# Kernel optimization log

Hardware: AMD Instinct MI355X
Metric: run time of the kernel (lower is better)

Reference implementation:

```python
import jax, jax.numpy as jnp
import numpy as np

B, HW, E = 64, 14, 512   # batch, feature-map side, encoder_dim
A = D = M = 512          # attention_dim, decoder_dim, embed_dim
V = 1000                 # vocab_size
L = 257                  # max caption length -> T = 256 decode steps


def setup_inputs() -> dict:
    key = jax.random.key(0)
    ks = jax.random.split(key, 16)
    def w(k, shape, s=0.05):
        return jax.random.normal(k, shape, dtype=jnp.float32) * s
    encoder_out = jax.random.normal(ks[0], (B, HW, HW, E), dtype=jnp.float32)
    encoded_captions = jax.random.randint(ks[1], (B, L), 0, V)
    caption_lengths = jax.random.randint(ks[2], (B, 1), 2, L + 1)
    caption_lengths = caption_lengths.at[0, 0].set(L)  # ensure max(decode_lengths) == L-1
    return dict(
        encoder_out=encoder_out,
        encoded_captions=encoded_captions,
        caption_lengths=caption_lengths,
        emb=w(ks[3], (V, M), 0.1),
        enc_att_w=w(ks[4], (A, E)), enc_att_b=jnp.zeros((A,), jnp.float32),
        dec_att_w=w(ks[5], (A, D)), dec_att_b=jnp.zeros((A,), jnp.float32),
        full_att_w=w(ks[6], (1, A)), full_att_b=jnp.zeros((1,), jnp.float32),
        W_ih=w(ks[7], (4 * D, M + E)), b_ih=jnp.zeros((4 * D,), jnp.float32),
        W_hh=w(ks[8], (4 * D, D)), b_hh=jnp.zeros((4 * D,), jnp.float32),
        init_h_w=w(ks[9], (D, E)), init_h_b=jnp.zeros((D,), jnp.float32),
        init_c_w=w(ks[10], (D, E)), init_c_b=jnp.zeros((D,), jnp.float32),
        f_beta_w=w(ks[11], (E, D)), f_beta_b=jnp.zeros((E,), jnp.float32),
        fc_w=w(ks[12], (V, D), 0.1), fc_b=jnp.zeros((V,), jnp.float32),
    )


def _forward(encoder_out, emb, enc_att_w, enc_att_b, dec_att_w, dec_att_b,
             full_att_w, full_att_b, W_ih, b_ih, W_hh, b_hh,
             init_h_w, init_h_b, init_c_w, init_c_b,
             f_beta_w, f_beta_b, fc_w, fc_b,
             encoded_captions, caption_lengths):
    Bn = encoder_out.shape[0]
    En = encoder_out.shape[-1]
    enc = encoder_out.reshape(Bn, -1, En)            # [B, P, E]
    lens = caption_lengths[:, 0]
    sort_ind = jnp.argsort(-lens)                    # descending caption length
    lens = lens[sort_ind]
    enc = enc[sort_ind]
    caps = encoded_captions[sort_ind]
    embs = emb[caps]                                 # [B, L, M]
    mean_enc = enc.mean(axis=1)
    h0 = mean_enc @ init_h_w.T + init_h_b            # [B, D]
    c0 = mean_enc @ init_c_w.T + init_c_b
    att1 = enc @ enc_att_w.T + enc_att_b             # [B, P, A] (loop-invariant)
    dec_len = lens - 1
    T = caps.shape[1] - 1
    embs_seq = jnp.transpose(embs[:, :T, :], (1, 0, 2))  # [T, B, M]

    def step(carry, xs):
        h, c = carry
        t, emb_t = xs
        # soft attention (full batch; torch slices to active rows, masked below)
        att2 = h @ dec_att_w.T + dec_att_b                                   # [B, A]
        e = jnp.einsum('bpa,a->bp', jax.nn.relu(att1 + att2[:, None, :]),
                       full_att_w[0]) + full_att_b[0]                        # [B, P]
        alpha = jax.nn.softmax(e, axis=1)
        awe = jnp.einsum('bpe,bp->be', enc, alpha)                           # [B, E]
        gate = jax.nn.sigmoid(h @ f_beta_w.T + f_beta_b)
        x = jnp.concatenate([emb_t, gate * awe], axis=1)                     # [B, M+E]
        # LSTMCell
        gates = x @ W_ih.T + b_ih + h @ W_hh.T + b_hh
        i, f, g, o = jnp.split(gates, 4, axis=1)
        c_new = jax.nn.sigmoid(f) * c + jax.nn.sigmoid(i) * jnp.tanh(g)
        h_new = jax.nn.sigmoid(o) * jnp.tanh(c_new)
        m = (t < dec_len).astype(h.dtype)[:, None]                           # active mask
        h2 = m * h_new + (1 - m) * h
        c2 = m * c_new + (1 - m) * c
        preds = (h_new @ fc_w.T + fc_b) * m   # dropout is identity in eval
        return (h2, c2), (preds, alpha * m)

    (_, _), (preds, alphas) = jax.lax.scan(step, (h0, c0), (jnp.arange(T), embs_seq))
    predictions = jnp.transpose(preds, (1, 0, 2))   # [B, T, V]
    alphas = jnp.transpose(alphas, (1, 0, 2))       # [B, T, P]
    return predictions, caps, alphas, sort_ind


def reference(encoder_out, encoded_captions, caption_lengths, emb,
              enc_att_w, enc_att_b, dec_att_w, dec_att_b, full_att_w, full_att_b,
              W_ih, b_ih, W_hh, b_hh, init_h_w, init_h_b, init_c_w, init_c_b,
              f_beta_w, f_beta_b, fc_w, fc_b):
    return _forward(encoder_out, emb, enc_att_w, enc_att_b, dec_att_w, dec_att_b,
                    full_att_w, full_att_b, W_ih, b_ih, W_hh, b_hh,
                    init_h_w, init_h_b, init_c_w, init_c_b,
                    f_beta_w, f_beta_b, fc_w, fc_b,
                    encoded_captions, caption_lengths)
```

## Files before the change

kernel.cpp:

```cpp
#include <hip/hip_runtime.h>
#include <cstdint>
#include <cstddef>

#define NBLK 256
#define NTHR 512
#define B_ 64
#define P_ 196
#define E_ 512
#define A_ 512
#define D_ 512
#define M_ 512
#define V_ 1000
#define L_ 257
#define T_ 256

#define OUT_PRED  0
#define OUT_CAPS  (B_*T_*V_)
#define OUT_ALPHA (OUT_CAPS + B_*L_)
#define OUT_SORT  (OUT_ALPHA + B_*T_*P_)

typedef _Float16 h2 __attribute__((ext_vector_type(2)));
typedef _Float16 f16x8 __attribute__((ext_vector_type(8)));
typedef float f32x4 __attribute__((ext_vector_type(4)));

struct KP {
  const float* enc; const int* caps; const int* clen;
  const float* emb;
  const float* eaw; const float* eab;
  const float* daw; const float* dab;
  const float* faw; const float* fab;
  const float* wih; const float* bih;
  const float* whh; const float* bhh;
  const float* ihw; const float* ihb;
  const float* icw; const float* icb;
  const float* fbw; const float* fbb;
  const float* fcw; const float* fcb;
  float* out;
  int* bar; int* flb; int* gf;
  int* sort_ind; int* dec_len;
  float* mnT;
  unsigned* hfA; unsigned* hfB; unsigned* hfN;
  float* a2G; float* gateG; float* aweQ; float* sA; float* att1;
};

__device__ __forceinline__ float sigf(float x){ return 1.f/(1.f+__expf(-x)); }
__device__ __forceinline__ float tanhf_(float x){
  float ax = fabsf(x);
  float e = __expf(-2.f*ax);
  float r = (1.f-e)/(1.f+e);
  return x < 0.f ? -r : r;
}
__device__ __forceinline__ unsigned short f2bf(float x){
  unsigned u = __float_as_uint(x);
  unsigned r = (u + 0x7fffu + ((u >> 16) & 1u)) >> 16;
  return (unsigned short)r;
}
__device__ __forceinline__ float fdot2f(h2 a, h2 b, float c){
#if __has_builtin(__builtin_amdgcn_fdot2)
  return __builtin_amdgcn_fdot2(a, b, c, false);
#else
  return c + (float)a.x*(float)b.x + (float)a.y*(float)b.y;
#endif
}
__device__ __forceinline__ unsigned packh2(float a, float b){
  h2 v; v.x = (_Float16)a; v.y = (_Float16)b;
  return __builtin_bit_cast(unsigned, v);
}
__device__ __forceinline__ h2 ash2(unsigned u){ return __builtin_bit_cast(h2, u); }
__device__ __forceinline__ f16x8 asf8(uint4 u){ return __builtin_bit_cast(f16x8, u); }

#define LD_A(p)     __hip_atomic_load((p), __ATOMIC_RELAXED, __HIP_MEMORY_SCOPE_AGENT)
#define ST_A(p,v)   __hip_atomic_store((p),(v), __ATOMIC_RELAXED, __HIP_MEMORY_SCOPE_AGENT)
#define ST_REL(p,v) __hip_atomic_store((p),(v), __ATOMIC_RELEASE, __HIP_MEMORY_SCOPE_AGENT)
#define FAA(p)      __hip_atomic_fetch_add((p),1, __ATOMIC_RELAXED, __HIP_MEMORY_SCOPE_AGENT)
__device__ __forceinline__ float ldg_c(const float* p){
  return __hip_atomic_load(p, __ATOMIC_RELAXED, __HIP_MEMORY_SCOPE_AGENT);
}
__device__ __forceinline__ float2 ldg2_c(const float* p){
  unsigned long long u = __hip_atomic_load((const unsigned long long*)p,
                       __ATOMIC_RELAXED, __HIP_MEMORY_SCOPE_AGENT);
  return __builtin_bit_cast(float2, u);
}
__device__ __forceinline__ uint2 ldgu2_c(const unsigned* p){
  unsigned long long u = __hip_atomic_load((const unsigned long long*)p,
                       __ATOMIC_RELAXED, __HIP_MEMORY_SCOPE_AGENT);
  return __builtin_bit_cast(uint2, u);
}
__device__ __forceinline__ void stg_c(float* p, float v){
  __hip_atomic_store(p, v, __ATOMIC_RELAXED, __HIP_MEMORY_SCOPE_AGENT);
}
__device__ __forceinline__ void stgu_c(unsigned* p, unsigned v){
  __hip_atomic_store(p, v, __ATOMIC_RELAXED, __HIP_MEMORY_SCOPE_AGENT);
}
__device__ __forceinline__ void stg2_c(float* p, float a, float b){
  float2 v; v.x = a; v.y = b;
  __hip_atomic_store((unsigned long long*)p,
                     __builtin_bit_cast(unsigned long long, v),
                     __ATOMIC_RELAXED, __HIP_MEMORY_SCOPE_AGENT);
}

__device__ __forceinline__ void gridbar(int* bar, int blk){
  __syncthreads();
  if (threadIdx.x == 0){
    __builtin_amdgcn_fence(__ATOMIC_RELEASE, "agent");
    int s = LD_A(&bar[144]);
    int* leaf = &bar[(blk & 7)*16];
    if (FAA(leaf) == 31){
      ST_A(leaf, 0);
      if (FAA(&bar[128]) == 7){
        ST_A(&bar[128], 0);
        ST_REL(&bar[144], s+1);
      }
    }
    while (LD_A(&bar[144]) == s) __builtin_amdgcn_s_sleep(2);
    __builtin_amdgcn_fence(__ATOMIC_ACQUIRE, "agent");
  }
  __syncthreads();
}

__device__ __forceinline__ void octbar(int* fl, int O, int r, int ep){
  __syncthreads();
  if (threadIdx.x == 0) ST_A(&fl[O*64 + r], ep);
  if (threadIdx.x < 32){
    while (LD_A(&fl[O*64 + (int)threadIdx.x]) < ep) __builtin_amdgcn_s_sleep(1);
  }
  asm volatile("" ::: "memory");
  __syncthreads();
}

#define REDW_STORE() do { \
  const int j = lane & 15; \
  if (j < 8){ \
    const int ib = (lane >> 4) * 4; \
    _Pragma("unroll") \
    for (int r = 0; r < 4; r++){ \
      redW[wave*512 + (( 0 + ib + r)*8) + j] = d0[r]; \
      redW[wave*512 + ((16 + ib + r)*8) + j] = d1[r]; \
      redW[wave*512 + ((32 + ib + r)*8) + j] = d2[r]; \
      redW[wave*512 + ((48 + ib + r)*8) + j] = d3[r]; \
    } \
  } \
} while(0)

template<int KSW>
__device__ __forceinline__ void gemv_regs(const uint4 (&wfr)[4][KSW],
                                          const uint4* __restrict__ x4,
                                          float* redW, int lane, int wave){
  f32x4 d0 = {0.f,0.f,0.f,0.f}, d1 = d0, d2 = d0, d3 = d0;
  const int rowc = lane & 7;
  const int lg = lane >> 4;
  #pragma unroll
  for (int ks = 0; ks < KSW; ks++){
    const int ksg = wave*KSW + ks;
    f16x8 bf = asf8(x4[(ksg*4 + lg)*8 + rowc]);
    d0 = __builtin_amdgcn_mfma_f32_16x16x32_f16(asf8(wfr[0][ks]), bf, d0, 0, 0, 0);
    d1 = __builtin_amdgcn_mfma_f32_16x16x32_f16(asf8(wfr[1][ks]), bf, d1, 0, 0, 0);
    d2 = __builtin_amdgcn_mfma_f32_16x16x32_f16(asf8(wfr[2][ks]), bf, d2, 0, 0, 0);
    d3 = __builtin_amdgcn_mfma_f32_16x16x32_f16(asf8(wfr[3][ks]), bf, d3, 0, 0, 0);
  }
  REDW_STORE();
}

__device__ __forceinline__ void gemv_dir2(const uint4 (&wfr)[4][2],
                                          const unsigned* __restrict__ hsrc,
                                          float* redW, int lane, int wave){
  f32x4 d0 = {0.f,0.f,0.f,0.f}, d1 = d0, d2 = d0, d3 = d0;
  const int rowc = lane & 7;
  const int lg = lane >> 4;
  #pragma unroll
  for (int ks = 0; ks < 2; ks++){
    const int ksg = wave*2 + ks;
    const unsigned* ad = hsrc + (rowc << 8) + ((ksg*4 + lg) << 2);
    uint2 u0 = ldgu2_c(ad), u1 = ldgu2_c(ad + 2);
    uint4 br; br.x = u0.x; br.y = u0.y; br.z = u1.x; br.w = u1.y;
    f16x8 bf = asf8(br);
    d0 = __builtin_amdgcn_mfma_f32_16x16x32_f16(asf8(wfr[0][ks]), bf, d0, 0, 0, 0);
    d1 = __builtin_amdgcn_mfma_f32_16x16x32_f16(asf8(wfr[1][ks]), bf, d1, 0, 0, 0);
    d2 = __builtin_amdgcn_mfma_f32_16x16x32_f16(asf8(wfr[2][ks]), bf, d2, 0, 0, 0);
    d3 = __builtin_amdgcn_mfma_f32_16x16x32_f16(asf8(wfr[3][ks]), bf, d3, 0, 0, 0);
  }
  REDW_STORE();
}

__global__ __launch_bounds__(NTHR, 2) void dec_kernel(KP p){
  __shared__ __align__(16) char smem_raw[152320];
  unsigned short* att1L = (unsigned short*)smem_raw;
  unsigned* encT2  = (unsigned*)(smem_raw + 50176);
  float* fwL       = (float*)(smem_raw + 105472);
  float* cL        = (float*)(smem_raw + 107520);
  int*   sbL       = (int*)(smem_raw + 108032);
  float* hLoc      = (float*)(smem_raw + 108096);
  float* hnT       = (float*)(smem_raw + 108608);
  char* SCR        = smem_raw + 109312;
  uint4* xH8_4     = (uint4*)SCR;
  float* redW      = (float*)(SCR + 24576);
  float* gLs       = (float*)(SCR + 40960);
  float* a2L       = (float*)SCR;
  float* gateL     = (float*)(SCR + 2048);
  float* eL        = (float*)(SCR + 4096);
  float* alphaL    = (float*)(SCR + 4352);
  unsigned* alpha2L= (unsigned*)(SCR + 4608);

  const int blk  = blockIdx.x;
  const int tid  = threadIdx.x;
  const int lane = tid & 63;
  const int wave = tid >> 6;
  const int b    = blk >> 2;
  const int q    = blk & 3;
  const int ct   = blk & 31;
  const int bt   = blk >> 5;

  if (blk == 0){
    if (tid < B_){
      int lb = p.clen[tid];
      int rank = 0;
      for (int j = 0; j < B_; j++){
        int lj = p.clen[j];
        rank += (lj > lb) || (lj == lb && j < tid);
      }
      p.sort_ind[rank] = tid;
      p.dec_len[rank]  = lb - 1;
      p.out[OUT_SORT + rank] = (float)tid;
    }
    __syncthreads();
    for (int idx = tid; idx < B_*L_; idx += NTHR){
      int bb = idx / L_;
      int l = idx - bb*L_;
      int sbv = p.sort_ind[bb];
      p.out[OUT_CAPS + idx] = (float)p.caps[sbv*L_ + l];
    }
  }
  gridbar(p.bar, blk);

  const int sb  = p.sort_ind[b];
  const int dlb = p.dec_len[b];

  for (int task = blk; task < 260; task += NBLK){
    if (task < 196){
      const int r0 = task*64;
      float* wL = (float*)smem_raw;
      float* eLt = (float*)smem_raw + 512*33;
      const int tx = tid & 31, ty = tid >> 5;
      float acc[4][16];
      #pragma unroll
      for (int i=0;i<4;i++)
        #pragma unroll
        for (int j=0;j<16;j++) acc[i][j] = 0.f;
      for (int k0 = 0; k0 < 512; k0 += 32){
        __syncthreads();
        for (int i = tid; i < 512*32; i += NTHR){
          int a = i >> 5, kk = i & 31;
          wL[a*33 + kk] = p.eaw[a*512 + k0 + kk];
        }
        for (int i = tid; i < 64*32; i += NTHR){
          int rl = i >> 5, kk = i & 31;
          int r = r0 + rl;
          int bb = r / 196;
          int pp = r - bb*196;
          int sbv = p.sort_ind[bb];
          eLt[rl*33 + kk] = p.enc[((size_t)sbv*196 + pp)*512 + k0 + kk];
        }
        __syncthreads();
        for (int kk = 0; kk < 32; kk++){
          float ev[4];
          #pragma unroll
          for (int ii=0;ii<4;ii++) ev[ii] = eLt[(ty*4+ii)*33 + kk];
          #pragma unroll
          for (int jj=0;jj<16;jj++){
            float wv = wL[(tx + 32*jj)*33 + kk];
            #pragma unroll
            for (int ii=0;ii<4;ii++) acc[ii][jj] = fmaf(ev[ii], wv, acc[ii][jj]);
          }
        }
      }
      #pragma unroll
      for (int jj=0;jj<16;jj++){
        int a = tx + 32*jj;
        float bbv = p.eab[a];
        #pragma unroll
        for (int ii=0;ii<4;ii++){
          int r = r0 + ty*4 + ii;
          p.att1[(size_t)r*512 + a] = acc[ii][jj] + bbv;
        }
      }
      __syncthreads();
    } else {
      int bb = task - 196;
      int sbv = p.sort_ind[bb];
      const float* eb = p.enc + (size_t)sbv*P_*E_;
      for (int e = tid; e < E_; e += NTHR){
        float s = 0.f;
        for (int pp = 0; pp < P_; pp++) s += eb[pp*E_ + e];
        p.mnT[bb*512 + e] = s * (1.f/196.f);
      }
    }
  }
  gridbar(p.bar, blk);

  for (int idx = tid; idx < 49*512; idx += NTHR){
    int pp = idx >> 9, a = idx & 511;
    att1L[idx] = f2bf(p.att1[((size_t)(b*196 + q*49 + pp))*512 + a]);
  }
  for (int i = tid; i < 512*25; i += NTHR){
    int p2 = i >> 9, e = i & 511;
    int pr0 = q*49 + 2*p2;
    float e0 = p.enc[((size_t)sb*196 + pr0)*512 + e];
    float e1 = (2*p2+1 < 49) ? p.enc[((size_t)sb*196 + pr0 + 1)*512 + e] : 0.f;
    encT2[e*27 + p2] = packh2(e0, e1);
  }
  fwL[tid] = p.faw[tid];
  if (tid < 8)       sbL[tid]     = p.sort_ind[bt*8 + tid];
  else if (tid < 16) sbL[tid]     = p.dec_len[bt*8 + (tid-8)];
  uint4 wa[4][2];
  uint4 wg[4][6];
  {
    const int cgb = ct*64 + (lane & 15);
    const int kof = (lane >> 4) << 3;
    #pragma unroll
    for (int mt = 0; mt < 4; mt++){
      int cg = cgb + mt*16;
      #pragma unroll
      for (int ks = 0; ks < 2; ks++){
        int k = (wave*2 + ks)*32 + kof;
        uint4 o = {0u,0u,0u,0u};
        const float* src = nullptr;
        if (cg < 512)        src = p.daw + (size_t)cg*512 + k;
        else if (cg < 1024)  src = p.fbw + (size_t)(cg-512)*512 + k;
        else if (cg < 2024)  src = p.fcw + (size_t)(cg-1024)*512 + k;
        if (src){
          const float4* s4 = (const float4*)src;
          float4 f0 = s4[0], f1 = s4[1];
          o.x = packh2(f0.x,f0.y); o.y = packh2(f0.z,f0.w);
          o.z = packh2(f1.x,f1.y); o.w = packh2(f1.z,f1.w);
        }
        wa[mt][ks] = o;
      }
      int jj = cg >> 2, g = cg & 3;
      #pragma unroll
      for (int ks = 0; ks < 6; ks++){
        int k = (wave*6 + ks)*32 + kof;
        const float* src = (k < 1024) ? p.wih + (size_t)(g*512+jj)*1024 + k
                                      : p.whh + (size_t)(g*512+jj)*512 + (k-1024);
        const float4* s4 = (const float4*)src;
        float4 f0 = s4[0], f1 = s4[1];
        uint4 o;
        o.x = packh2(f0.x,f0.y); o.y = packh2(f0.z,f0.w);
        o.z = packh2(f1.x,f1.y); o.w = packh2(f1.z,f1.w);
        wg[mt][ks] = o;
      }
    }
  }
  if (tid < 128){
    int jj = tid >> 3, bb2 = tid & 7;
    int b8 = bt*8 + bb2, jg = ct*16 + jj;
    const float* mrow = p.mnT + b8*512;
    const float* hw = p.ihw + (size_t)jg*512;
    const float* cw = p.icw + (size_t)jg*512;
    float ah = 0.f, ac = 0.f;
    for (int k = 0; k < 512; k++){ ah = fmaf(hw[k], mrow[k], ah); ac = fmaf(cw[k], mrow[k], ac); }
    hLoc[jj*8 + bb2] = ah + p.ihb[jg];
    cL[jj*8 + bb2] = ac + p.icb[jg];
  }
  __syncthreads();
  if (tid < 64){
    int j2 = tid >> 3, bb2 = tid & 7;
    int b8 = bt*8 + bb2;
    stgu_c(&p.hfA[b8*256 + ct*8 + j2],
           packh2(hLoc[(2*j2)*8 + bb2], hLoc[(2*j2+1)*8 + bb2]));
  }
  gridbar(p.bar, blk);

  const float fab0 = p.fab[0];
  int ep = 0;

  for (int t = 0; t < T_; t++){
    const unsigned* hfR = (t & 1) ? p.hfB : p.hfA;
    unsigned*       hfW = (t & 1) ? p.hfA : p.hfB;

    uint4 embPre;
    {
      int cc = tid >> 3, r = tid & 7;
      int cap = p.caps[sbL[r]*L_ + t];
      const float4* er = (const float4*)(p.emb + (size_t)cap*M_ + cc*8);
      float4 f0 = er[0], f1 = er[1];
      embPre.x = packh2(f0.x,f0.y); embPre.y = packh2(f0.z,f0.w);
      embPre.z = packh2(f1.x,f1.y); embPre.w = packh2(f1.z,f1.w);
    }

    if (ct < 16 || t > 0){
      const unsigned* xsrc = ((ct < 16) ? hfR : p.hfN) + bt*8*256;
      gemv_dir2(wa, xsrc, redW, lane, wave);
      __syncthreads();
      {
        float s = 0.f;
        #pragma unroll
        for (int w8 = 0; w8 < 8; w8++) s += redW[w8*512 + tid];
        int c_local = tid >> 3, j = tid & 7, b8 = bt*8 + j;
        if (ct < 16){
          int vcl = ct*64 + c_local;
          if (vcl < 512) stg_c(&p.a2G[b8*512 + vcl], s + p.dab[vcl]);
          else           stg_c(&p.gateG[b8*512 + (vcl-512)], sigf(s + p.fbb[vcl-512]));
        } else {
          int v2i = (ct-16)*64 + c_local;
          if (v2i < 1000){
            bool mm = (t-1) < sbL[8 + j];
            p.out[OUT_PRED + ((size_t)b8*T_ + (t-1))*V_ + v2i] = mm ? (s + p.fcb[v2i]) : 0.f;
          }
        }
      }
    }
    octbar(p.flb, bt, ct, ++ep);

    {
      a2L[tid]   = ldg_c(&p.a2G[b*512 + tid]);
      gateL[tid] = ldg_c(&p.gateG[b*512 + tid]);
      __syncthreads();
      {
        float4 aA = ((float4*)a2L)[lane*2], aB = ((float4*)a2L)[lane*2+1];
        float4 fA = ((float4*)fwL)[lane*2], fB = ((float4*)fwL)[lane*2+1];
        for (int pp = wave; pp < 49; pp += 8){
          uint4 raw = ((const uint4*)att1L)[pp*64 + lane];
          float s =
            fmaxf(__uint_as_float(raw.x << 16)        + aA.x, 0.f)*fA.x +
            fmaxf(__uint_as_float(raw.x & 0xffff0000u)+ aA.y, 0.f)*fA.y +
            fmaxf(__uint_as_float(raw.y << 16)        + aA.z, 0.f)*fA.z +
            fmaxf(__uint_as_float(raw.y & 0xffff0000u)+ aA.w, 0.f)*fA.w +
            fmaxf(__uint_as_float(raw.z << 16)        + aB.x, 0.f)*fB.x +
            fmaxf(__uint_as_float(raw.z & 0xffff0000u)+ aB.y, 0.f)*fB.y +
            fmaxf(__uint_as_float(raw.w << 16)        + aB.z, 0.f)*fB.z +
            fmaxf(__uint_as_float(raw.w & 0xffff0000u)+ aB.w, 0.f)*fB.w;
          #pragma unroll
          for (int o = 32; o > 0; o >>= 1) s += __shfl_down(s, o);
          if (lane == 0) eL[pp] = s + fab0;
        }
      }
      __syncthreads();
      float l_ex = 0.f, l_mx = -1e30f;
      if (wave == 0){
        float ev = (lane < 49) ? eL[lane] : -1e30f;
        l_mx = ev;
        #pragma unroll
        for (int o = 32; o > 0; o >>= 1) l_mx = fmaxf(l_mx, __shfl_xor(l_mx, o));
        l_ex = (lane < 49) ? __expf(ev - l_mx) : 0.f;
        float sum = l_ex;
        #pragma unroll
        for (int o = 32; o > 0; o >>= 1) sum += __shfl_xor(sum, o);
        if (lane == 0) stg2_c(&p.sA[(b*4 + q)*2], l_mx, sum);
      }
      __syncthreads();
      if (tid == 0) ST_A(&p.gf[b*16 + q], t+1);
      if (tid < 4){
        while (LD_A(&p.gf[b*16 + tid]) < t+1) __builtin_amdgcn_s_sleep(1);
      }
      asm volatile("" ::: "memory");
      __syncthreads();
      if (wave == 0){
        float2 s0 = ldg2_c(&p.sA[(b*4 + 0)*2]);
        float2 s1 = ldg2_c(&p.sA[(b*4 + 1)*2]);
        float2 s2 = ldg2_c(&p.sA[(b*4 + 2)*2]);
        float2 s3 = ldg2_c(&p.sA[(b*4 + 3)*2]);
        float gmx = fmaxf(fmaxf(s0.x, s1.x), fmaxf(s2.x, s3.x));
        float gsum = s0.y*__expf(s0.x - gmx) + s1.y*__expf(s1.x - gmx)
                   + s2.y*__expf(s2.x - gmx) + s3.y*__expf(s3.x - gmx);
        float r = __expf(l_mx - gmx) / gsum;
        if (lane < 49){
          float al = l_ex * r;
          alphaL[lane] = al;
          p.out[OUT_ALPHA + ((size_t)b*T_ + t)*P_ + q*49 + lane] = (t < dlb) ? al : 0.f;
        }
      }
      __syncthreads();
      if (tid < 25){
        float a0 = alphaL[2*tid];
        float a1 = (2*tid+1 < 49) ? alphaL[2*tid + 1] : 0.f;
        alpha2L[tid] = packh2(a0, a1);
      }
      __syncthreads();
      {
        const unsigned* ec = encT2 + tid*27;
        float s = 0.f;
        #pragma unroll 5
        for (int p2 = 0; p2 < 25; p2++)
          s = fdot2f(ash2(ec[p2]), ash2(alpha2L[p2]), s);
        stg_c(&p.aweQ[((size_t)b*4 + q)*512 + tid], gateL[tid]*s);
      }
    }
    octbar(p.flb, bt, ct, ++ep);

    {
      {
        int cc = tid >> 3, r = tid & 7;
        int b8 = bt*8 + r;
        xH8_4[tid] = embPre;
        const unsigned* hs = hfR + b8*256 + cc*4;
        uint2 u0 = ldgu2_c(hs), u1 = ldgu2_c(hs + 2);
        uint4 o; o.x = u0.x; o.y = u0.y; o.z = u1.x; o.w = u1.y;
        xH8_4[1024 + tid] = o;
        const float* aw = p.aweQ + (size_t)b8*4*512 + cc*8;
        float a8[8];
        #pragma unroll
        for (int e = 0; e < 8; e += 2){
          float2 q0 = ldg2_c(aw + 0*512 + e);
          float2 q1 = ldg2_c(aw + 1*512 + e);
          float2 q2 = ldg2_c(aw + 2*512 + e);
          float2 q3 = ldg2_c(aw + 3*512 + e);
          a8[e]   = (q0.x + q1.x) + (q2.x + q3.x);
          a8[e+1] = (q0.y + q1.y) + (q2.y + q3.y);
        }
        uint4 ow;
        ow.x = packh2(a8[0],a8[1]); ow.y = packh2(a8[2],a8[3]);
        ow.z = packh2(a8[4],a8[5]); ow.w = packh2(a8[6],a8[7]);
        xH8_4[512 + tid] = ow;
      }
      __syncthreads();
      gemv_regs<6>(wg, xH8_4, redW, lane, wave);
      __syncthreads();
      {
        float s = 0.f;
        #pragma unroll
        for (int w8 = 0; w8 < 8; w8++) s += redW[w8*512 + tid];
        gLs[(tid & 7)*64 + (tid >> 3)] = s;
      }
      __syncthreads();
      if (tid < 128){
        int jj = tid >> 3, bb2 = tid & 7;
        int jg = ct*16 + jj;
        float g0 = gLs[bb2*64 + jj*4+0] + p.bih[jg]        + p.bhh[jg];
        float g1 = gLs[bb2*64 + jj*4+1] + p.bih[512 + jg]  + p.bhh[512 + jg];
        float g2 = gLs[bb2*64 + jj*4+2] + p.bih[1024 + jg] + p.bhh[1024 + jg];
        float g3 = gLs[bb2*64 + jj*4+3] + p.bih[1536 + jg] + p.bhh[1536 + jg];
        float i_s = sigf(g0), f_s = sigf(g1), g_t = tanhf_(g2), o_s = sigf(g3);
        float c_old = cL[jj*8 + bb2];
        float c_new = f_s*c_old + i_s*g_t;
        float h_new = o_s*tanhf_(c_new);
        bool m = t < sbL[8 + bb2];
        float h_old = hLoc[jj*8 + bb2];
        cL[jj*8 + bb2]   = m ? c_new : c_old;
        hLoc[jj*8 + bb2] = m ? h_new : h_old;
        hnT[jj*8 + bb2]  = h_new;
      }
      __syncthreads();
      if (tid < 64){
        int j2 = tid >> 3, bb2 = tid & 7;
        int b8 = bt*8 + bb2;
        stgu_c(&hfW[b8*256 + ct*8 + j2],
               packh2(hLoc[(2*j2)*8 + bb2], hLoc[(2*j2+1)*8 + bb2]));
        stgu_c(&p.hfN[b8*256 + ct*8 + j2],
               packh2(hnT[(2*j2)*8 + bb2], hnT[(2*j2+1)*8 + bb2]));
      }
    }
    octbar(p.flb, bt, ct, ++ep);
  }

  if (ct >= 16){
    gemv_dir2(wa, p.hfN + bt*8*256, redW, lane, wave);
    __syncthreads();
    {
      float s = 0.f;
      #pragma unroll
      for (int w8 = 0; w8 < 8; w8++) s += redW[w8*512 + tid];
      int c_local = tid >> 3, j = tid & 7, b8 = bt*8 + j;
      int v2i = (ct-16)*64 + c_local;
      if (v2i < 1000){
        bool mm = (T_-1) < sbL[8 + j];
        p.out[OUT_PRED + ((size_t)b8*T_ + (T_-1))*V_ + v2i] = mm ? (s + p.fcb[v2i]) : 0.f;
      }
    }
  }
}

extern "C" void kernel_launch(void* const* d_in, const int* in_sizes, int n_in,
                              void* d_out, int out_size, void* d_ws, size_t ws_size,
                              hipStream_t stream){
  (void)in_sizes; (void)n_in; (void)out_size; (void)ws_size;
  KP p;
  p.enc  = (const float*)d_in[0];
  p.caps = (const int*)  d_in[1];
  p.clen = (const int*)  d_in[2];
  p.emb  = (const float*)d_in[3];
  p.eaw  = (const float*)d_in[4];  p.eab = (const float*)d_in[5];
  p.daw  = (const float*)d_in[6];  p.dab = (const float*)d_in[7];
  p.faw  = (const float*)d_in[8];  p.fab = (const float*)d_in[9];
  p.wih  = (const float*)d_in[10]; p.bih = (const float*)d_in[11];
  p.whh  = (const float*)d_in[12]; p.bhh = (const float*)d_in[13];
  p.ihw  = (const float*)d_in[14]; p.ihb = (const float*)d_in[15];
  p.icw  = (const float*)d_in[16]; p.icb = (const float*)d_in[17];
  p.fbw  = (const float*)d_in[18]; p.fbb = (const float*)d_in[19];
  p.fcw  = (const float*)d_in[20]; p.fcb = (const float*)d_in[21];
  p.out  = (float*)d_out;

  char* ws = (char*)d_ws;
  size_t off = 0;
  p.bar = (int*)(ws + off); off += 1024;
  p.flb = (int*)(ws + off); off += 8*64*4;
  p.gf  = (int*)(ws + off); off += 64*16*4;
  size_t zero_bytes = off;
  p.sort_ind = (int*)(ws + off); off += 64*4;
  p.dec_len  = (int*)(ws + off); off += 64*4;
  off = (off + 255) & ~(size_t)255;
  p.mnT   = (float*)(ws + off); off += (size_t)B_*512*4;
  p.hfA   = (unsigned*)(ws + off); off += (size_t)B_*256*4;
  p.hfB   = (unsigned*)(ws + off); off += (size_t)B_*256*4;
  p.hfN   = (unsigned*)(ws + off); off += (size_t)B_*256*4;
  p.a2G   = (float*)(ws + off); off += (size_t)B_*512*4;
  p.gateG = (float*)(ws + off); off += (size_t)B_*512*4;
  p.aweQ  = (float*)(ws + off); off += (size_t)B_*4*512*4;
  p.sA    = (float*)(ws + off); off += (size_t)B_*4*2*4;
  off = (off + 255) & ~(size_t)255;
  p.att1  = (float*)(ws + off); off += (size_t)B_*P_*A_*4;

  hipMemsetAsync(ws, 0, zero_bytes, stream);

  void* args[] = { (void*)&p };
  hipLaunchCooperativeKernel((const void*)dec_kernel,
                             dim3(NBLK), dim3(NTHR), args, 0, stream);
}
```

Baseline: 5.324 ms.

## Keep LSTM state in registers and trim barriers in the attention phase

Moves the LSTM h/c state and the combined gate biases into registers, using cross-lane shuffles instead of shared-memory staging. This removes several __syncthreads per step. In the attention phase it computes the unnormalised alpha-weighted encoder sum before waiting on the cross-block softmax flag, then scales it by the global normalisation factor afterwards, so the flag spin overlaps with that dot product. Bias loads for the per-step outputs are hoisted out of the time loop. The risks are correctness of the shuffle lane mapping, slight precision differences from packing the unnormalised exponentials to fp16, and higher register pressure.

```diff
diff --git a/kernel.cpp b/kernel.cpp
--- a/kernel.cpp
+++ b/kernel.cpp
@@ -183,23 +183,16 @@
 }
 
 __global__ __launch_bounds__(NTHR, 2) void dec_kernel(KP p){
-  __shared__ __align__(16) char smem_raw[152320];
+  __shared__ __align__(16) char smem_raw[148544];
   unsigned short* att1L = (unsigned short*)smem_raw;
   unsigned* encT2  = (unsigned*)(smem_raw + 50176);
   float* fwL       = (float*)(smem_raw + 105472);
-  float* cL        = (float*)(smem_raw + 107520);
-  int*   sbL       = (int*)(smem_raw + 108032);
-  float* hLoc      = (float*)(smem_raw + 108096);
-  float* hnT       = (float*)(smem_raw + 108608);
-  char* SCR        = smem_raw + 109312;
+  int*   sbL       = (int*)(smem_raw + 107520);
+  char* SCR        = smem_raw + 107584;
   uint4* xH8_4     = (uint4*)SCR;
   float* redW      = (float*)(SCR + 24576);
-  float* gLs       = (float*)(SCR + 40960);
-  float* a2L       = (float*)SCR;
-  float* gateL     = (float*)(SCR + 2048);
-  float* eL        = (float*)(SCR + 4096);
-  float* alphaL    = (float*)(SCR + 4352);
-  unsigned* alpha2L= (unsigned*)(SCR + 4608);
+  float* eL        = (float*)SCR;
+  unsigned* alpha2L= (unsigned*)(SCR + 256);
 
   const int blk  = blockIdx.x;
   const int tid  = threadIdx.x;
@@ -350,23 +343,39 @@
       }
     }
   }
-  if (tid < 128){
-    int jj = tid >> 3, bb2 = tid & 7;
-    int b8 = bt*8 + bb2, jg = ct*16 + jj;
+  float hreg = 0.f, creg = 0.f;
+  float lb0 = 0.f, lb1 = 0.f, lb2 = 0.f, lb3 = 0.f;
+  const bool isLstm = (tid & 31) < 8;
+  if (isLstm){
+    int jl = tid >> 5, bb2 = tid & 7;
+    int b8 = bt*8 + bb2, jg = ct*16 + jl;
     const float* mrow = p.mnT + b8*512;
     const float* hw = p.ihw + (size_t)jg*512;
     const float* cw = p.icw + (size_t)jg*512;
     float ah = 0.f, ac = 0.f;
     for (int k = 0; k < 512; k++){ ah = fmaf(hw[k], mrow[k], ah); ac = fmaf(cw[k], mrow[k], ac); }
-    hLoc[jj*8 + bb2] = ah + p.ihb[jg];
-    cL[jj*8 + bb2] = ac + p.icb[jg];
-  }
-  __syncthreads();
-  if (tid < 64){
-    int j2 = tid >> 3, bb2 = tid & 7;
-    int b8 = bt*8 + bb2;
-    stgu_c(&p.hfA[b8*256 + ct*8 + j2],
-           packh2(hLoc[(2*j2)*8 + bb2], hLoc[(2*j2+1)*8 + bb2]));
+    hreg = ah + p.ihb[jg];
+    creg = ac + p.icb[jg];
+    lb0 = p.bih[jg]        + p.bhh[jg];
+    lb1 = p.bih[512 + jg]  + p.bhh[512 + jg];
+    lb2 = p.bih[1024 + jg] + p.bhh[1024 + jg];
+    lb3 = p.bih[1536 + jg] + p.bhh[1536 + jg];
+  }
+  {
+    float h1 = __shfl(hreg, lane + 32);
+    if (lane < 8)
+      stgu_c(&p.hfA[(bt*8 + lane)*256 + ct*8 + wave], packh2(hreg, h1));
+  }
+  float p1b = 0.f;
+  {
+    int c_local = tid >> 3;
+    if (ct < 16){
+      int vcl = ct*64 + c_local;
+      p1b = (vcl < 512) ? p.dab[vcl] : p.fbb[vcl - 512];
+    } else {
+      int v2i = (ct-16)*64 + c_local;
+      p1b = (v2i < 1000) ? p.fcb[v2i] : 0.f;
+    }
   }
   gridbar(p.bar, blk);
 
@@ -398,63 +407,82 @@
         int c_local = tid >> 3, j = tid & 7, b8 = bt*8 + j;
         if (ct < 16){
           int vcl = ct*64 + c_local;
-          if (vcl < 512) stg_c(&p.a2G[b8*512 + vcl], s + p.dab[vcl]);
-          else           stg_c(&p.gateG[b8*512 + (vcl-512)], sigf(s + p.fbb[vcl-512]));
+          if (vcl < 512) stg_c(&p.a2G[b8*512 + vcl], s + p1b);
+          else           stg_c(&p.gateG[b8*512 + (vcl-512)], sigf(s + p1b));
         } else {
           int v2i = (ct-16)*64 + c_local;
           if (v2i < 1000){
             bool mm = (t-1) < sbL[8 + j];
-            p.out[OUT_PRED + ((size_t)b8*T_ + (t-1))*V_ + v2i] = mm ? (s + p.fcb[v2i]) : 0.f;
+            p.out[OUT_PRED + ((size_t)b8*T_ + (t-1))*V_ + v2i] = mm ? (s + p1b) : 0.f;
           }
         }
       }
     }
     octbar(p.flb, bt, ct, ++ep);
 
+    float l_ex = 0.f, l_mx = -1e30f;
     {
-      a2L[tid]   = ldg_c(&p.a2G[b*512 + tid]);
-      gateL[tid] = ldg_c(&p.gateG[b*512 + tid]);
+      const float* a2p = p.a2G + b*512 + lane*8;
+      float2 aA0 = ldg2_c(a2p),     aA1 = ldg2_c(a2p + 2);
+      float2 aB0 = ldg2_c(a2p + 4), aB1 = ldg2_c(a2p + 6);
+      float gate_r = ldg_c(&p.gateG[b*512 + tid]);
+      float4 fA = ((float4*)fwL)[lane*2], fB = ((float4*)fwL)[lane*2+1];
+      for (int pp = wave; pp < 49; pp += 8){
+        uint4 raw = ((const uint4*)att1L)[pp*64 + lane];
+        float s =
+          fmaxf(__uint_as_float(raw.x << 16)        + aA0.x, 0.f)*fA.x +
+          fmaxf(__uint_as_float(raw.x & 0xffff0000u)+ aA0.y, 0.f)*fA.y +
+          fmaxf(__uint_as_float(raw.y << 16)        + aA1.x, 0.f)*fA.z +
+          fmaxf(__uint_as_float(raw.y & 0xffff0000u)+ aA1.y, 0.f)*fA.w +
+          fmaxf(__uint_as_float(raw.z << 16)        + aB0.x, 0.f)*fB.x +
+          fmaxf(__uint_as_float(raw.z & 0xffff0000u)+ aB0.y, 0.f)*fB.y +
+          fmaxf(__uint_as_float(raw.w << 16)        + aB1.x, 0.f)*fB.z +
+          fmaxf(__uint_as_float(raw.w & 0xffff0000u)+ aB1.y, 0.f)*fB.w;
+        #pragma unroll
+        for (int o = 32; o > 0; o >>= 1) s += __shfl_down(s, o);
+        if (lane == 0) eL[pp] = s + fab0;
+      }
       __syncthreads();
-      {
-        float4 aA = ((float4*)a2L)[lane*2], aB = ((float4*)a2L)[lane*2+1];
-        float4 fA = ((float4*)fwL)[lane*2], fB = ((float4*)fwL)[lane*2+1];
-        for (int pp = wave; pp < 49; pp += 8){
-          uint4 raw = ((const uint4*)att1L)[pp*64 + lane];
-          float s =
-            fmaxf(__uint_as_float(raw.x << 16)        + aA.x, 0.f)*fA.x +
-            fmaxf(__uint_as_float(raw.x & 0xffff0000u)+ aA.y, 0.f)*fA.y +
-            fmaxf(__uint_as_float(raw.y << 16)        + aA.z, 0.f)*fA.z +
-            fmaxf(__uint_as_float(raw.y & 0xffff0000u)+ aA.w, 0.f)*fA.w +
-            fmaxf(__uint_as_float(raw.z << 16)        + aB.x, 0.f)*fB.x +
-            fmaxf(__uint_as_float(raw.z & 0xffff0000u)+ aB.y, 0.f)*fB.y +
-            fmaxf(__uint_as_float(raw.w << 16)        + aB.z, 0.f)*fB.z +
-            fmaxf(__uint_as_float(raw.w & 0xffff0000u)+ aB.w, 0.f)*fB.w;
-          #pragma unroll
-          for (int o = 32; o > 0; o >>= 1) s += __shfl_down(s, o);
-          if (lane == 0) eL[pp] = s + fab0;
-        }
-      }
-      __syncthreads();
-      float l_ex = 0.f, l_mx = -1e30f;
       if (wave == 0){
         float ev = (lane < 49) ? eL[lane] : -1e30f;
         l_mx = ev;
         #pragma unroll
         for (int o = 32; o > 0; o >>= 1) l_mx = fmaxf(l_mx, __shfl_xor(l_mx, o));
         l_ex = (lane < 49) ? __expf(ev - l_mx) : 0.f;
+        float a0 = __shfl(l_ex, 2*lane);
+        float a1 = __shfl(l_ex, 2*lane + 1);
+        if (lane < 25) alpha2L[lane] = packh2(a0, a1);
         float sum = l_ex;
         #pragma unroll
         for (int o = 32; o > 0; o >>= 1) sum += __shfl_xor(sum, o);
-        if (lane == 0) stg2_c(&p.sA[(b*4 + q)*2], l_mx, sum);
+        if (lane == 0){
+          stg2_c(&p.sA[(b*4 + q)*2], l_mx, sum);
+          ST_REL(&p.gf[b*16 + q], t+1);
+        }
       }
       __syncthreads();
-      if (tid == 0) ST_A(&p.gf[b*16 + q], t+1);
-      if (tid < 4){
-        while (LD_A(&p.gf[b*16 + tid]) < t+1) __builtin_amdgcn_s_sleep(1);
-      }
-      asm volatile("" ::: "memory");
-      __syncthreads();
-      if (wave == 0){
+      float s = 0.f;
+      {
+        const unsigned* ec = encT2 + tid*27;
+        #pragma unroll 5
+        for (int p2 = 0; p2 < 25; p2++)
+          s = fdot2f(ash2(ec[p2]), ash2(alpha2L[p2]), s);
+      }
+      {
+        const unsigned long long* g0 = (const unsigned long long*)&p.gf[b*16];
+        int tt = t + 1;
+        while (true){
+          unsigned long long v0 = __hip_atomic_load(g0,     __ATOMIC_RELAXED, __HIP_MEMORY_SCOPE_AGENT);
+          unsigned long long v1 = __hip_atomic_load(g0 + 1, __ATOMIC_RELAXED, __HIP_MEMORY_SCOPE_AGENT);
+          int m0 = (int)(unsigned)v0, m1 = (int)(v0 >> 32);
+          int m2 = (int)(unsigned)v1, m3 = (int)(v1 >> 32);
+          if (m0 >= tt && m1 >= tt && m2 >= tt && m3 >= tt) break;
+          __builtin_amdgcn_s_sleep(1);
+        }
+        __builtin_amdgcn_fence(__ATOMIC_ACQUIRE, "agent");
+      }
+      float r;
+      {
         float2 s0 = ldg2_c(&p.sA[(b*4 + 0)*2]);
         float2 s1 = ldg2_c(&p.sA[(b*4 + 1)*2]);
         float2 s2 = ldg2_c(&p.sA[(b*4 + 2)*2]);
@@ -462,35 +490,19 @@
         float gmx = fmaxf(fmaxf(s0.x, s1.x), fmaxf(s2.x, s3.x));
         float gsum = s0.y*__expf(s0.x - gmx) + s1.y*__expf(s1.x - gmx)
                    + s2.y*__expf(s2.x - gmx) + s3.y*__expf(s3.x - gmx);
-        float r = __expf(l_mx - gmx) / gsum;
-        if (lane < 49){
-          float al = l_ex * r;
-          alphaL[lane] = al;
-          p.out[OUT_ALPHA + ((size_t)b*T_ + t)*P_ + q*49 + lane] = (t < dlb) ? al : 0.f;
-        }
-      }
-      __syncthreads();
-      if (tid < 25){
-        float a0 = alphaL[2*tid];
-        float a1 = (2*tid+1 < 49) ? alphaL[2*tid + 1] : 0.f;
-        alpha2L[tid] = packh2(a0, a1);
-      }
-      __syncthreads();
-      {
-        const unsigned* ec = encT2 + tid*27;
-        float s = 0.f;
-        #pragma unroll 5
-        for (int p2 = 0; p2 < 25; p2++)
-          s = fdot2f(ash2(ec[p2]), ash2(alpha2L[p2]), s);
-        stg_c(&p.aweQ[((size_t)b*4 + q)*512 + tid], gateL[tid]*s);
-      }
+        float mq = (q == 0) ? s0.x : (q == 1) ? s1.x : (q == 2) ? s2.x : s3.x;
+        r = __expf(mq - gmx) / gsum;
+      }
+      stg_c(&p.aweQ[((size_t)b*4 + q)*512 + tid], gate_r * s * r);
+      if (wave == 0 && lane < 49)
+        p.out[OUT_ALPHA + ((size_t)b*T_ + t)*P_ + q*49 + lane] = (t < dlb) ? l_ex*r : 0.f;
     }
     octbar(p.flb, bt, ct, ++ep);
 
     {
       {
-        int cc = tid >> 3, r = tid & 7;
-        int b8 = bt*8 + r;
+        int cc = tid >> 3, r8 = tid & 7;
+        int b8 = bt*8 + r8;
         xH8_4[tid] = embPre;
         const unsigned* hs = hfR + b8*256 + cc*4;
         uint2 u0 = ldgu2_c(hs), u1 = ldgu2_c(hs + 2);
@@ -515,38 +527,29 @@
       __syncthreads();
       gemv_regs<6>(wg, xH8_4, redW, lane, wave);
       __syncthreads();
-      {
-        float s = 0.f;
-        #pragma unroll
-        for (int w8 = 0; w8 < 8; w8++) s += redW[w8*512 + tid];
-        gLs[(tid & 7)*64 + (tid >> 3)] = s;
-      }
-      __syncthreads();
-      if (tid < 128){
-        int jj = tid >> 3, bb2 = tid & 7;
-        int jg = ct*16 + jj;
-        float g0 = gLs[bb2*64 + jj*4+0] + p.bih[jg]        + p.bhh[jg];
-        float g1 = gLs[bb2*64 + jj*4+1] + p.bih[512 + jg]  + p.bhh[512 + jg];
-        float g2 = gLs[bb2*64 + jj*4+2] + p.bih[1024 + jg] + p.bhh[1024 + jg];
-        float g3 = gLs[bb2*64 + jj*4+3] + p.bih[1536 + jg] + p.bhh[1536 + jg];
-        float i_s = sigf(g0), f_s = sigf(g1), g_t = tanhf_(g2), o_s = sigf(g3);
-        float c_old = cL[jj*8 + bb2];
-        float c_new = f_s*c_old + i_s*g_t;
-        float h_new = o_s*tanhf_(c_new);
+      float s = 0.f;
+      #pragma unroll
+      for (int w8 = 0; w8 < 8; w8++) s += redW[w8*512 + tid];
+      float g1 = __shfl(s, lane + 8);
+      float g2 = __shfl(s, lane + 16);
+      float g3 = __shfl(s, lane + 24);
+      float hnv = 0.f;
+      if (isLstm){
+        int bb2 = tid & 7;
+        float G0 = s  + lb0, G1 = g1 + lb1, G2 = g2 + lb2, G3 = g3 + lb3;
+        float i_s = sigf(G0), f_s = sigf(G1), g_t = tanhf_(G2), o_s = sigf(G3);
+        float c_new = f_s*creg + i_s*g_t;
+        hnv = o_s*tanhf_(c_new);
         bool m = t < sbL[8 + bb2];
-        float h_old = hLoc[jj*8 + bb2];
-        cL[jj*8 + bb2]   = m ? c_new : c_old;
-        hLoc[jj*8 + bb2] = m ? h_new : h_old;
-        hnT[jj*8 + bb2]  = h_new;
-      }
-      __syncthreads();
-      if (tid < 64){
-        int j2 = tid >> 3, bb2 = tid & 7;
-        int b8 = bt*8 + bb2;
-        stgu_c(&hfW[b8*256 + ct*8 + j2],
-               packh2(hLoc[(2*j2)*8 + bb2], hLoc[(2*j2+1)*8 + bb2]));
-        stgu_c(&p.hfN[b8*256 + ct*8 + j2],
-               packh2(hnT[(2*j2)*8 + bb2], hnT[(2*j2+1)*8 + bb2]));
+        creg = m ? c_new : creg;
+        hreg = m ? hnv  : hreg;
+      }
+      float hm1 = __shfl(hreg, lane + 32);
+      float hn1 = __shfl(hnv,  lane + 32);
+      if (lane < 8){
+        int b8 = bt*8 + lane;
+        stgu_c(&hfW[b8*256 + ct*8 + wave],    packh2(hreg, hm1));
+        stgu_c(&p.hfN[b8*256 + ct*8 + wave],  packh2(hnv,  hn1));
       }
     }
     octbar(p.flb, bt, ct, ++ep);
@@ -563,7 +566,7 @@
       int v2i = (ct-16)*64 + c_local;
       if (v2i < 1000){
         bool mm = (T_-1) < sbL[8 + j];
-        p.out[OUT_PRED + ((size_t)b8*T_ + (T_-1))*V_ + v2i] = mm ? (s + p.fcb[v2i]) : 0.f;
+        p.out[OUT_PRED + ((size_t)b8*T_ + (T_-1))*V_ + v2i] = mm ? (s + p1b) : 0.f;
       }
     }
   }
```

Measured after the change: 8.434 ms. +58.4%, slower.
